# Kernel optimization log

Hardware: AMD Instinct MI355X
Metric: run time of the kernel (lower is better)

The kernel has to match this reference:

```python
import jax, jax.numpy as jnp
import numpy as np

B, H, DK, DV = 64, 32, 128, 128


def setup_inputs() -> dict:
    key = jax.random.key(0)
    ks = jax.random.split(key, 6)
    return {
        "S": jax.random.normal(ks[0], (B, H, DK, DV), dtype=jnp.float32),
        "k": jax.random.normal(ks[1], (B, H, DK), dtype=jnp.float32),
        "v": jax.random.normal(ks[2], (B, H, DV), dtype=jnp.float32),
        "q": jax.random.normal(ks[3], (B, H, DK), dtype=jnp.float32),
        "alpha": jax.random.uniform(ks[4], (B, H, DK), dtype=jnp.float32),
        "beta": jax.random.uniform(ks[5], (B, H, 1), dtype=jnp.float32),
    }


def reference(S, k, v, q, alpha, beta):
    # S_t = (I - beta k k^T) Diag(alpha) S_{t-1} + beta k v^T ;  o_t = S_t^T q
    S_decay = alpha[..., None] * S                              # (B,H,dk,dv)
    kT_S = jnp.einsum('bhd,bhdv->bhv', k, S_decay)              # k^T (Diag(a) S)
    kkT_S = k[..., :, None] * kT_S[..., None, :]                # outer(k, k^T S)
    kvT = k[..., :, None] * v[..., None, :]                     # outer(k, v)
    S_new = S_decay - beta[..., None] * kkT_S + beta[..., None] * kvT
    o = jnp.einsum('bhdv,bhd->bhv', S_new, q)
    return (S_new, o)
```

## Files before the change

kernel.cpp:

```cpp
#include <hip/hip_runtime.h>


#define DK 128
#define DV 128

__global__ __launch_bounds__(256) void kda_update_kernel(
    const float* __restrict__ S,
    const float* __restrict__ k,
    const float* __restrict__ v,
    const float* __restrict__ q,
    const float* __restrict__ alpha,
    const float* __restrict__ beta,
    float* __restrict__ Sout,
    float* __restrict__ o)
{
    const int bh   = blockIdx.x;
    const int tid  = threadIdx.x;
    const int col4 = (tid & 31) * 4;
    const int rgrp = tid >> 5;

    __shared__ float sk[DK];
    __shared__ float sa[DK];
    __shared__ float sq[DK];
    __shared__ float scoef[DV];
    __shared__ float red[8][DV];

    const size_t head_off = (size_t)bh * DK * DV;
    const float* __restrict__ Sbh = S + head_off;

    if (tid < DK) {
        sk[tid] = k[(size_t)bh * DK + tid];
        sa[tid] = alpha[(size_t)bh * DK + tid];
        sq[tid] = q[(size_t)bh * DK + tid];
    }
    __syncthreads();

    float s_reg[16][4];
    float part0 = 0.f, part1 = 0.f, part2 = 0.f, part3 = 0.f;
    const int d0 = rgrp * 16;

    #pragma unroll
    for (int i = 0; i < 16; ++i) {
        const int d = d0 + i;
        const float4 sv = *reinterpret_cast<const float4*>(Sbh + (size_t)d * DV + col4);
        s_reg[i][0] = sv.x; s_reg[i][1] = sv.y; s_reg[i][2] = sv.z; s_reg[i][3] = sv.w;
        const float ak = sa[d] * sk[d];
        part0 += ak * sv.x;
        part1 += ak * sv.y;
        part2 += ak * sv.z;
        part3 += ak * sv.w;
    }

    red[rgrp][col4 + 0] = part0;
    red[rgrp][col4 + 1] = part1;
    red[rgrp][col4 + 2] = part2;
    red[rgrp][col4 + 3] = part3;
    __syncthreads();

    if (tid < DV) {
        float s = 0.f;
        #pragma unroll
        for (int g = 0; g < 8; ++g) s += red[g][tid];
        const float b = beta[bh];
        scoef[tid] = b * (v[(size_t)bh * DV + tid] - s);
    }
    __syncthreads();

    const float c0 = scoef[col4 + 0];
    const float c1 = scoef[col4 + 1];
    const float c2 = scoef[col4 + 2];
    const float c3 = scoef[col4 + 3];

    float o0 = 0.f, o1 = 0.f, o2 = 0.f, o3 = 0.f;
    float* __restrict__ Sobh = Sout + head_off;

    #pragma unroll
    for (int i = 0; i < 16; ++i) {
        const int d = d0 + i;
        const float a  = sa[d];
        const float kk = sk[d];
        const float qq = sq[d];
        float4 ov;
        ov.x = a * s_reg[i][0] + kk * c0;
        ov.y = a * s_reg[i][1] + kk * c1;
        ov.z = a * s_reg[i][2] + kk * c2;
        ov.w = a * s_reg[i][3] + kk * c3;
        *reinterpret_cast<float4*>(Sobh + (size_t)d * DV + col4) = ov;
        o0 += qq * ov.x;
        o1 += qq * ov.y;
        o2 += qq * ov.z;
        o3 += qq * ov.w;
    }

    red[rgrp][col4 + 0] = o0;
    red[rgrp][col4 + 1] = o1;
    red[rgrp][col4 + 2] = o2;
    red[rgrp][col4 + 3] = o3;
    __syncthreads();

    if (tid < DV) {
        float s = 0.f;
        #pragma unroll
        for (int g = 0; g < 8; ++g) s += red[g][tid];
        o[(size_t)bh * DV + tid] = s;
    }
}

extern "C" void kernel_launch(void* const* d_in, const int* in_sizes, int n_in,
                              void* d_out, int out_size, void* d_ws, size_t ws_size,
                              hipStream_t stream) {
    const float* S     = (const float*)d_in[0];
    const float* k     = (const float*)d_in[1];
    const float* v     = (const float*)d_in[2];
    const float* q     = (const float*)d_in[3];
    const float* alpha = (const float*)d_in[4];
    const float* beta  = (const float*)d_in[5];

    const int BH = in_sizes[5];

    float* Sout = (float*)d_out;
    float* o    = Sout + (size_t)BH * DK * DV;

    kda_update_kernel<<<dim3(BH), dim3(256), 0, stream>>>(S, k, v, q, alpha, beta, Sout, o);
}
```

Measured before the change: 50.86 us.

## Assign one thread per value column to remove shared-memory reductions

The kernel now uses 128 threads per head. Each thread owns one full column of S (128 floats held in registers), so both reductions over dk happen within a single thread and the shared-memory reduction buffers and extra barriers go away. Loads become scalar but still coalesced across the warp, stores use nontemporal hints, and alpha*k is precomputed into shared memory. The cost is very high register pressure (128 floats per thread, possible spills) and half as many threads per block, which cuts memory-level parallelism for this bandwidth-bound update.

```diff
diff --git a/kernel.cpp b/kernel.cpp
--- a/kernel.cpp
+++ b/kernel.cpp
@@ -4,7 +4,7 @@
 #define DK 128
 #define DV 128
 
-__global__ __launch_bounds__(256) void kda_update_kernel(
+__global__ __launch_bounds__(128) void kda_update_kernel(
     const float* __restrict__ S,
     const float* __restrict__ k,
     const float* __restrict__ v,
@@ -14,96 +14,47 @@
     float* __restrict__ Sout,
     float* __restrict__ o)
 {
-    const int bh   = blockIdx.x;
-    const int tid  = threadIdx.x;
-    const int col4 = (tid & 31) * 4;
-    const int rgrp = tid >> 5;
+    const int bh = blockIdx.x;
+    const int e  = threadIdx.x;
 
+    __shared__ float sak[DK];
+    __shared__ float sa[DK];
     __shared__ float sk[DK];
-    __shared__ float sa[DK];
     __shared__ float sq[DK];
-    __shared__ float scoef[DV];
-    __shared__ float red[8][DV];
 
-    const size_t head_off = (size_t)bh * DK * DV;
-    const float* __restrict__ Sbh = S + head_off;
+    const size_t hoff = (size_t)bh * DK * DV;
+    const float* __restrict__ Sbh = S + hoff;
 
-    if (tid < DK) {
-        sk[tid] = k[(size_t)bh * DK + tid];
-        sa[tid] = alpha[(size_t)bh * DK + tid];
-        sq[tid] = q[(size_t)bh * DK + tid];
+    {
+        const float kk = k[(size_t)bh * DK + e];
+        const float aa = alpha[(size_t)bh * DK + e];
+        sk[e]  = kk;
+        sa[e]  = aa;
+        sak[e] = kk * aa;
+        sq[e]  = q[(size_t)bh * DK + e];
     }
     __syncthreads();
 
-    float s_reg[16][4];
-    float part0 = 0.f, part1 = 0.f, part2 = 0.f, part3 = 0.f;
-    const int d0 = rgrp * 16;
-
+    float s_col[DK];
+    float kts = 0.f;
     #pragma unroll
-    for (int i = 0; i < 16; ++i) {
-        const int d = d0 + i;
-        const float4 sv = *reinterpret_cast<const float4*>(Sbh + (size_t)d * DV + col4);
-        s_reg[i][0] = sv.x; s_reg[i][1] = sv.y; s_reg[i][2] = sv.z; s_reg[i][3] = sv.w;
-        const float ak = sa[d] * sk[d];
-        part0 += ak * sv.x;
-        part1 += ak * sv.y;
-        part2 += ak * sv.z;
-        part3 += ak * sv.w;
+    for (int d = 0; d < DK; ++d) {
+        s_col[d] = Sbh[(size_t)d * DV + e];
+        kts += sak[d] * s_col[d];
     }
 
-    red[rgrp][col4 + 0] = part0;
-    red[rgrp][col4 + 1] = part1;
-    red[rgrp][col4 + 2] = part2;
-    red[rgrp][col4 + 3] = part3;
-    __syncthreads();
+    const float coef = beta[bh] * (v[(size_t)bh * DV + e] - kts);
 
-    if (tid < DV) {
-        float s = 0.f;
-        #pragma unroll
-        for (int g = 0; g < 8; ++g) s += red[g][tid];
-        const float b = beta[bh];
-        scoef[tid] = b * (v[(size_t)bh * DV + tid] - s);
-    }
-    __syncthreads();
-
-    const float c0 = scoef[col4 + 0];
-    const float c1 = scoef[col4 + 1];
-    const float c2 = scoef[col4 + 2];
-    const float c3 = scoef[col4 + 3];
-
-    float o0 = 0.f, o1 = 0.f, o2 = 0.f, o3 = 0.f;
-    float* __restrict__ Sobh = Sout + head_off;
-
+    float oacc = 0.f;
+    float* __restrict__ Sobh = Sout + hoff;
     #pragma unroll
-    for (int i = 0; i < 16; ++i) {
-        const int d = d0 + i;
-        const float a  = sa[d];
-        const float kk = sk[d];
-        const float qq = sq[d];
-        float4 ov;
-        ov.x = a * s_reg[i][0] + kk * c0;
-        ov.y = a * s_reg[i][1] + kk * c1;
-        ov.z = a * s_reg[i][2] + kk * c2;
-        ov.w = a * s_reg[i][3] + kk * c3;
-        *reinterpret_cast<float4*>(Sobh + (size_t)d * DV + col4) = ov;
-        o0 += qq * ov.x;
-        o1 += qq * ov.y;
-        o2 += qq * ov.z;
-        o3 += qq * ov.w;
+    for (int d = 0; d < DK; ++d) {
+        const float sn = sa[d] * s_col[d] + sk[d] * coef;
+        __builtin_nontemporal_store(sn, Sobh + (size_t)d * DV + e);
+        oacc += sq[d] * sn;
     }
 
-    red[rgrp][col4 + 0] = o0;
-    red[rgrp][col4 + 1] = o1;
-    red[rgrp][col4 + 2] = o2;
-    red[rgrp][col4 + 3] = o3;
-    __syncthreads();
-
-    if (tid < DV) {
-        float s = 0.f;
-        #pragma unroll
-        for (int g = 0; g < 8; ++g) s += red[g][tid];
-        o[(size_t)bh * DV + tid] = s;
-    }
+    o[(size_t)bh * DV + e] = oacc;
 }
 
 extern "C" void kernel_launch(void* const* d_in, const int* in_sizes, int n_in,
@@ -121,5 +72,5 @@
     float* Sout = (float*)d_out;
     float* o    = Sout + (size_t)BH * DK * DV;
 
-    kda_update_kernel<<<dim3(BH), dim3(256), 0, stream>>>(S, k, v, q, alpha, beta, Sout, o);
+    kda_update_kernel<<<dim3(BH), dim3(128), 0, stream>>>(S, k, v, q, alpha, beta, Sout, o);
 }
```

Result: faster. 44.47 us (-12.6%).
